# Kernel tuning notes

Hardware: AMD Instinct MI355X
Metric: run time of the kernel (lower is better)

The kernel has to match this reference:

```python
import jax, jax.numpy as jnp
import numpy as np

S, D, H, F = 4096, 1024, 16, 4096
DH = D // H  # 64
EPS = 1e-6


def _layer_norm(x, scale, bias):
    mu = jnp.mean(x, axis=-1, keepdims=True)
    var = jnp.mean(jnp.square(x - mu), axis=-1, keepdims=True)
    return (x - mu) * jax.lax.rsqrt(var + EPS) * scale + bias


def setup_inputs() -> dict:
    key = jax.random.key(0)
    ks = jax.random.split(key, 12)
    s = 0.02
    return {
        "x": jax.random.normal(ks[0], (S, D), jnp.float32),
        "Wq": jax.random.normal(ks[1], (D, H, DH), jnp.float32) * s,
        "bq": jnp.zeros((H, DH), jnp.float32),
        "Wk": jax.random.normal(ks[2], (D, H, DH), jnp.float32) * s,
        "bk": jnp.zeros((H, DH), jnp.float32),
        "Wv": jax.random.normal(ks[3], (D, H, DH), jnp.float32) * s,
        "bv": jnp.zeros((H, DH), jnp.float32),
        "Wo": jax.random.normal(ks[4], (H, DH, D), jnp.float32) * s,
        "bo": jnp.zeros((D,), jnp.float32),
        "ln1_scale": jnp.ones((D,), jnp.float32),
        "ln1_bias": jnp.zeros((D,), jnp.float32),
        "ln2_scale": jnp.ones((D,), jnp.float32),
        "ln2_bias": jnp.zeros((D,), jnp.float32),
        "W1": jax.random.normal(ks[5], (D, F), jnp.float32) * s,
        "b1": jnp.zeros((F,), jnp.float32),
        "W2": jax.random.normal(ks[6], (F, D), jnp.float32) * s,
        "b2": jnp.zeros((D,), jnp.float32),
    }


def reference(x, Wq, bq, Wk, bk, Wv, bv, Wo, bo,
              ln1_scale, ln1_bias, ln2_scale, ln2_bias,
              W1, b1, W2, b2):
    # --- attention block (pre-LN, no mask, no dropout, no RoPE) ---
    y = _layer_norm(x, ln1_scale, ln1_bias)            # [S, D]
    q = jnp.einsum("sd,dhk->shk", y, Wq) + bq          # [S, H, DH]
    k = jnp.einsum("sd,dhk->shk", y, Wk) + bk
    v = jnp.einsum("sd,dhk->shk", y, Wv) + bv
    scale = jnp.float32(1.0 / np.sqrt(DH))
    scores = jnp.einsum("qhd,khd->hqk", q * scale, k)  # [H, S, S]
    w = jax.nn.softmax(scores, axis=-1)
    ctx = jnp.einsum("hqk,khd->qhd", w, v)             # [S, H, DH]
    attn_out = jnp.einsum("qhd,hdo->qo", ctx, Wo) + bo  # [S, D]
    x = x + attn_out
    # --- FFN block ---
    y = _layer_norm(x, ln2_scale, ln2_bias)
    y = jax.nn.gelu(y @ W1 + b1, approximate=False)
    y = y @ W2 + b2
    return x + y
```

## Files before the change

### kernel.cpp

```cpp
#include <hip/hip_runtime.h>
#include <cstdint>
#include <cstddef>


typedef __attribute__((ext_vector_type(8))) __bf16 bf16x8;
typedef __attribute__((ext_vector_type(4))) float f32x4;
typedef __attribute__((ext_vector_type(2))) float f32x2;
typedef __attribute__((ext_vector_type(16))) float f32x16;
typedef __attribute__((ext_vector_type(4))) unsigned int u32x4;

__device__ inline unsigned short f2bf(float f) {
  unsigned int u = __float_as_uint(f);
  u += 0x7fffu + ((u >> 16) & 1u);
  return (unsigned short)(u >> 16);
}

__device__ inline void gload_lds16(const unsigned short* g, unsigned short* l) {
  __builtin_amdgcn_global_load_lds(
      (const __attribute__((address_space(1))) void*)g,
      (__attribute__((address_space(3))) void*)l, 16, 0, 0);
}

__global__ __launch_bounds__(256) void transpose_cvt(const float* __restrict__ in,
                                                     unsigned short* __restrict__ out,
                                                     int K, int N) {
  __shared__ float t[32][33];
  int nb = blockIdx.x * 32, kb = blockIdx.y * 32;
  int tx = threadIdx.x & 31, ty = threadIdx.x >> 5;
#pragma unroll
  for (int i = 0; i < 32; i += 8)
    t[ty + i][tx] = in[(size_t)(kb + ty + i) * N + nb + tx];
  __syncthreads();
#pragma unroll
  for (int i = 0; i < 32; i += 8)
    out[(size_t)(nb + ty + i) * K + kb + tx] = f2bf(t[tx][ty + i]);
}

__global__ __launch_bounds__(256) void concat3(const float* __restrict__ a,
                                               const float* __restrict__ b,
                                               const float* __restrict__ c,
                                               float* __restrict__ out) {
  int i = blockIdx.x * 256 + threadIdx.x;
  float v = (i < 1024) ? a[i] : (i < 2048 ? b[i - 1024] : c[i - 2048]);
  out[i] = v;
}

__global__ __launch_bounds__(256) void ln_kernel(const float* __restrict__ x,
                                                 const float* __restrict__ gamma,
                                                 const float* __restrict__ beta,
                                                 unsigned short* __restrict__ y) {
  int row = blockIdx.x, tid = threadIdx.x;
  const float4 v = ((const float4*)(x + (size_t)row * 1024))[tid];
  float s = v.x + v.y + v.z + v.w;
#pragma unroll
  for (int off = 1; off < 64; off <<= 1) s += __shfl_xor(s, off);
  __shared__ float red1[4], red2[4];
  int wave = tid >> 6;
  if ((tid & 63) == 0) red1[wave] = s;
  __syncthreads();
  float mu = (red1[0] + red1[1] + red1[2] + red1[3]) * (1.0f / 1024.0f);
  float dx = v.x - mu, dy = v.y - mu, dz = v.z - mu, dw = v.w - mu;
  float s2 = dx * dx + dy * dy + dz * dz + dw * dw;
#pragma unroll
  for (int off = 1; off < 64; off <<= 1) s2 += __shfl_xor(s2, off);
  if ((tid & 63) == 0) red2[wave] = s2;
  __syncthreads();
  float var = (red2[0] + red2[1] + red2[2] + red2[3]) * (1.0f / 1024.0f);
  float inv = rsqrtf(var + 1e-6f);
  int c = tid * 4;
  ushort4 o;
  o.x = f2bf(dx * inv * gamma[c + 0] + beta[c + 0]);
  o.y = f2bf(dy * inv * gamma[c + 1] + beta[c + 1]);
  o.z = f2bf(dz * inv * gamma[c + 2] + beta[c + 2]);
  o.w = f2bf(dw * inv * gamma[c + 3] + beta[c + 3]);
  ((ushort4*)(y + (size_t)row * 1024))[tid] = o;
}

template <int TM, bool GELU, bool RES, bool OUTBF, bool SCALEQ>
__global__ __launch_bounds__(256) void gemm_bt(const unsigned short* __restrict__ A,
                                               const unsigned short* __restrict__ BT,
                                               const float* __restrict__ bias,
                                               const float* __restrict__ res,
                                               void* __restrict__ out,
                                               int M, int N, int K) {
  constexpr int AI = TM / 32;
  __shared__ unsigned short As[TM * 32];
  __shared__ unsigned short Bs[128 * 32];
  int bm = blockIdx.x, bn = blockIdx.y;
  int tid = threadIdx.x;
  int wave = tid >> 6, lane = tid & 63, quad = lane >> 4, l16 = lane & 15;
  int wrow = (wave >> 1) * (16 * AI), wcol = (wave & 1) * 64;
  f32x4 zero = {0.f, 0.f, 0.f, 0.f};
  f32x4 acc[AI][4];
#pragma unroll
  for (int i = 0; i < AI; i++)
#pragma unroll
    for (int j = 0; j < 4; j++) acc[i][j] = zero;

  const int srow = tid >> 2;
  const int scol = (tid & 3) * 8;
  const unsigned short* aG0 = A + (size_t)(bm * TM + srow) * K + scol;
  const unsigned short* aG1 = A + (size_t)(bm * TM + 64 + srow) * K + scol;
  const unsigned short* bG0 = BT + (size_t)(bn * 128 + srow) * K + scol;
  const unsigned short* bG1 = BT + (size_t)(bn * 128 + 64 + srow) * K + scol;
  unsigned short* aL0 = As + (size_t)tid * 8;
  unsigned short* aL1 = As + (size_t)(256 + tid) * 8;
  unsigned short* bL0 = Bs + (size_t)tid * 8;
  unsigned short* bL1 = Bs + (size_t)(256 + tid) * 8;

  for (int k0 = 0; k0 < K; k0 += 32) {
    __syncthreads();
    gload_lds16(aG0 + k0, aL0);
    if (TM == 128) gload_lds16(aG1 + k0, aL1);
    gload_lds16(bG0 + k0, bL0);
    gload_lds16(bG1 + k0, bL1);
    __syncthreads();
    bf16x8 af[AI], bfr[4];
#pragma unroll
    for (int i = 0; i < AI; i++) af[i] = *(const bf16x8*)&As[(wrow + i * 16 + l16) * 32 + quad * 8];
#pragma unroll
    for (int j = 0; j < 4; j++) bfr[j] = *(const bf16x8*)&Bs[(wcol + j * 16 + l16) * 32 + quad * 8];
#pragma unroll
    for (int i = 0; i < AI; i++)
#pragma unroll
      for (int j = 0; j < 4; j++)
        acc[i][j] = __builtin_amdgcn_mfma_f32_16x16x32_bf16(af[i], bfr[j], acc[i][j], 0, 0, 0);
  }

#pragma unroll
  for (int i = 0; i < AI; i++) {
    int row = bm * TM + wrow + i * 16 + quad * 4;
#pragma unroll
    for (int j = 0; j < 4; j++) {
      int col = bn * 128 + wcol + j * 16 + l16;
      float bv = bias[col];
      float qs = (SCALEQ && col < 1024) ? 0.18033688f : 1.0f;
#pragma unroll
      for (int r = 0; r < 4; r++) {
        float v = (acc[i][j][r] + bv) * qs;
        if (GELU) v = 0.5f * v * (1.0f + erff(v * 0.70710678118654752440f));
        if (RES) v += res[(size_t)(row + r) * N + col];
        if (OUTBF)
          ((unsigned short*)out)[(size_t)(row + r) * N + col] = f2bf(v);
        else
          ((float*)out)[(size_t)(row + r) * N + col] = v;
      }
    }
  }
}

__global__ __launch_bounds__(256) void prep_kv(const unsigned short* __restrict__ qkv,
                                               unsigned short* __restrict__ Kp,
                                               unsigned short* __restrict__ Vp) {
  __shared__ unsigned short Vt[64 * 64];
  int t = blockIdx.x, h = blockIdx.y;
  int tid = threadIdx.x;
  const int r2 = tid >> 3, c0 = (tid & 7) * 8;
  size_t tb = ((size_t)h * 64 + t) * 4096;
  {
    const unsigned short* kp = qkv + (size_t)(t * 64 + r2) * 3072 + 1024 + h * 64 + c0;
    uint4 k0 = *(const uint4*)kp;
    uint4 k1 = *(const uint4*)(kp + (size_t)32 * 3072);
    int c = c0 >> 3;
    *(uint4*)(Kp + tb + c * 512 + r2 * 8) = k0;
    *(uint4*)(Kp + tb + c * 512 + (r2 + 32) * 8) = k1;
  }
  {
    const unsigned short* vp = qkv + (size_t)(t * 64 + 2 * r2) * 3072 + 2048 + h * 64 + c0;
    uint4 v0 = *(const uint4*)vp;
    uint4 v1 = *(const uint4*)(vp + 3072);
    const unsigned short* p0 = (const unsigned short*)&v0;
    const unsigned short* p1 = (const unsigned short*)&v1;
#pragma unroll
    for (int dd = 0; dd < 8; dd++) {
      unsigned int pk = (unsigned int)p0[dd] | ((unsigned int)p1[dd] << 16);
      *(unsigned int*)&Vt[(c0 + dd) * 64 + 2 * r2] = pk;
    }
  }
  __syncthreads();
#pragma unroll
  for (int u0 = 0; u0 < 2; u0++) {
    int u = tid + u0 * 256;
    *(uint4*)(Vp + tb + u * 8) = *(const uint4*)&Vt[(u & 63) * 64 + (u >> 6) * 8];
  }
}

__global__ __launch_bounds__(256, 3) void attn_kernel(const unsigned short* __restrict__ qkv,
                                                      const unsigned short* __restrict__ Kp,
                                                      const unsigned short* __restrict__ Vp,
                                                      unsigned short* __restrict__ ctx) {
  __shared__ float comb[2 * 32 * 64];
  __shared__ float lpart[4 * 32];
  int qt = blockIdx.x, h = blockIdx.y;
  int tid = threadIdx.x;
  int w = tid >> 6, lane = tid & 63;
  int l31 = lane & 31, hi = lane >> 5;
  int qsub = w & 1, kvh = w >> 1;

  bf16x8 qf[4];
  {
    const unsigned short* qp = qkv + (size_t)(qt * 64 + qsub * 32 + l31) * 3072 + h * 64 + hi * 8;
#pragma unroll
    for (int kk = 0; kk < 4; kk++) qf[kk] = *(const bf16x8*)(qp + kk * 16);
  }

  const size_t hb = (size_t)h * 64 * 4096;
  const unsigned short* kB = Kp + hb + hi * 512 + (kvh * 32 + l31) * 8;
  const unsigned short* vB = Vp + hb + (kvh * 4 + hi) * 512 + l31 * 8;

  f32x16 accO0, accO1;
  f32x2 lp2 = {0.f, 0.f};
#pragma unroll
  for (int r = 0; r < 16; r++) { accO0[r] = 0.f; accO1[r] = 0.f; }

  bf16x8 kf[4];
#pragma unroll
  for (int kk = 0; kk < 4; kk++) kf[kk] = *(const bf16x8*)(kB + kk * 1024);

  for (int t = 0; t < 64; t++) {
    const unsigned short* vt = vB + (size_t)t * 4096;
    bf16x8 vA0 = *(const bf16x8*)(vt);
    bf16x8 vA1 = *(const bf16x8*)(vt + 1024);
    bf16x8 vB0 = *(const bf16x8*)(vt + 256);
    bf16x8 vB1 = *(const bf16x8*)(vt + 1024 + 256);

    f32x16 accS;
#pragma unroll
    for (int r = 0; r < 16; r++) accS[r] = 0.f;
#pragma unroll
    for (int kk = 0; kk < 4; kk++)
      accS = __builtin_amdgcn_mfma_f32_32x32x16_bf16(kf[kk], qf[kk], accS, 0, 0, 0);

    if (t < 63) {
      const unsigned short* kt = kB + (size_t)(t + 1) * 4096;
#pragma unroll
      for (int kk = 0; kk < 4; kk++) kf[kk] = *(const bf16x8*)(kt + kk * 1024);
    }

    unsigned int pd[8];
#pragma unroll
    for (int i = 0; i < 8; i++) {
      float a = __builtin_amdgcn_exp2f(accS[2 * i]);
      float b = __builtin_amdgcn_exp2f(accS[2 * i + 1]);
      f32x2 ab = {a, b};
      lp2 += ab;
      pd[i] = __builtin_amdgcn_perm(__float_as_uint(b), __float_as_uint(a), 0x07060302);
    }
    asm("v_permlane32_swap_b32 %0, %1" : "+v"(pd[0]), "+v"(pd[2]));
    asm("v_permlane32_swap_b32 %0, %1" : "+v"(pd[1]), "+v"(pd[3]));
    asm("v_permlane32_swap_b32 %0, %1" : "+v"(pd[4]), "+v"(pd[6]));
    asm("v_permlane32_swap_b32 %0, %1" : "+v"(pd[5]), "+v"(pd[7]));
    u32x4 f0 = {pd[0], pd[1], pd[2], pd[3]};
    u32x4 f1 = {pd[4], pd[5], pd[6], pd[7]};
    bf16x8 pa0 = __builtin_bit_cast(bf16x8, f0);
    bf16x8 pa1 = __builtin_bit_cast(bf16x8, f1);

    accO0 = __builtin_amdgcn_mfma_f32_32x32x16_bf16(pa0, vA0, accO0, 0, 0, 0);
    accO1 = __builtin_amdgcn_mfma_f32_32x32x16_bf16(pa0, vB0, accO1, 0, 0, 0);
    accO0 = __builtin_amdgcn_mfma_f32_32x32x16_bf16(pa1, vA1, accO0, 0, 0, 0);
    accO1 = __builtin_amdgcn_mfma_f32_32x32x16_bf16(pa1, vB1, accO1, 0, 0, 0);
  }

  float lp = lp2.x + lp2.y;
  lp += __shfl_xor(lp, 32);
  if (hi == 0) lpart[(kvh * 2 + qsub) * 32 + l31] = lp;
  if (kvh == 1) {
#pragma unroll
    for (int r = 0; r < 16; r++) {
      int q = (r & 3) + 8 * (r >> 2) + 4 * hi;
      comb[(qsub * 32 + q) * 64 + l31] = accO0[r];
      comb[(qsub * 32 + q) * 64 + 32 + l31] = accO1[r];
    }
  }
  __syncthreads();
  if (kvh == 0) {
#pragma unroll
    for (int r = 0; r < 16; r++) {
      int q = (r & 3) + 8 * (r >> 2) + 4 * hi;
      float l = lpart[qsub * 32 + q] + lpart[(2 + qsub) * 32 + q];
      float inv = 1.0f / l;
      float v0 = (accO0[r] + comb[(qsub * 32 + q) * 64 + l31]) * inv;
      float v1 = (accO1[r] + comb[(qsub * 32 + q) * 64 + 32 + l31]) * inv;
      int row = qt * 64 + qsub * 32 + q;
      size_t o = (size_t)row * 1024 + h * 64;
      ctx[o + l31] = f2bf(v0);
      ctx[o + 32 + l31] = f2bf(v1);
    }
  }
}

extern "C" void kernel_launch(void* const* d_in, const int* in_sizes, int n_in,
                              void* d_out, int out_size, void* d_ws, size_t ws_size,
                              hipStream_t stream) {
  const float* x   = (const float*)d_in[0];
  const float* Wq  = (const float*)d_in[1];
  const float* bq  = (const float*)d_in[2];
  const float* Wk  = (const float*)d_in[3];
  const float* bk  = (const float*)d_in[4];
  const float* Wv  = (const float*)d_in[5];
  const float* bv  = (const float*)d_in[6];
  const float* Wo  = (const float*)d_in[7];
  const float* bo  = (const float*)d_in[8];
  const float* g1  = (const float*)d_in[9];
  const float* be1 = (const float*)d_in[10];
  const float* g2  = (const float*)d_in[11];
  const float* be2 = (const float*)d_in[12];
  const float* W1  = (const float*)d_in[13];
  const float* b1  = (const float*)d_in[14];
  const float* W2  = (const float*)d_in[15];
  const float* b2  = (const float*)d_in[16];
  float* out = (float*)d_out;

  char* p = (char*)d_ws;
  unsigned short* WqkvT = (unsigned short*)p; p += (size_t)3072 * 1024 * 2;
  unsigned short* WoT   = (unsigned short*)p; p += (size_t)1024 * 1024 * 2;
  unsigned short* W1T   = (unsigned short*)p; p += (size_t)4096 * 1024 * 2;
  unsigned short* W2T   = (unsigned short*)p; p += (size_t)1024 * 4096 * 2;
  float*          bqkv  = (float*)p;          p += 16384;
  unsigned short* y1    = (unsigned short*)p; p += (size_t)4096 * 1024 * 2;
  unsigned short* qkvb  = (unsigned short*)p; p += (size_t)4096 * 3072 * 2;
  unsigned short* ctxb  = (unsigned short*)p; p += (size_t)4096 * 1024 * 2;
  float*          x1    = (float*)p;          p += (size_t)4096 * 1024 * 4;
  unsigned short* Kp    = (unsigned short*)p; p += (size_t)16 * 64 * 4096 * 2;
  unsigned short* Vp    = (unsigned short*)p; p += (size_t)16 * 64 * 4096 * 2;
  unsigned short* hbuf  = qkvb;

  dim3 b256(256);
  transpose_cvt<<<dim3(32, 32), b256, 0, stream>>>(Wq, WqkvT, 1024, 1024);
  transpose_cvt<<<dim3(32, 32), b256, 0, stream>>>(Wk, WqkvT + (size_t)1024 * 1024, 1024, 1024);
  transpose_cvt<<<dim3(32, 32), b256, 0, stream>>>(Wv, WqkvT + (size_t)2048 * 1024, 1024, 1024);
  transpose_cvt<<<dim3(32, 32), b256, 0, stream>>>(Wo, WoT, 1024, 1024);
  transpose_cvt<<<dim3(128, 32), b256, 0, stream>>>(W1, W1T, 1024, 4096);
  transpose_cvt<<<dim3(32, 128), b256, 0, stream>>>(W2, W2T, 4096, 1024);
  concat3<<<12, b256, 0, stream>>>(bq, bk, bv, bqkv);

  ln_kernel<<<4096, b256, 0, stream>>>(x, g1, be1, y1);
  gemm_bt<128, false, false, true, true><<<dim3(32, 24), b256, 0, stream>>>(y1, WqkvT, bqkv, nullptr, qkvb, 4096, 3072, 1024);
  prep_kv<<<dim3(64, 16), b256, 0, stream>>>(qkvb, Kp, Vp);
  attn_kernel<<<dim3(64, 16), b256, 0, stream>>>(qkvb, Kp, Vp, ctxb);
  gemm_bt<64, false, true, false, false><<<dim3(64, 8), b256, 0, stream>>>(ctxb, WoT, bo, x, x1, 4096, 1024, 1024);
  ln_kernel<<<4096, b256, 0, stream>>>(x1, g2, be2, y1);
  gemm_bt<128, true, false, true, false><<<dim3(32, 32), b256, 0, stream>>>(y1, W1T, b1, nullptr, hbuf, 4096, 4096, 1024);
  gemm_bt<64, false, true, false, false><<<dim3(64, 8), b256, 0, stream>>>(hbuf, W2T, b2, x1, out, 4096, 1024, 4096);
}
```

Baseline: 446.1 us.

## Replace GEMM kernel with 8-wave double-buffered swizzled large-tile GEMM

Replaces the single-buffered 256-thread GEMM with a 512-thread kernel that uses larger tiles (256x256 or 128x128) and BK=64. It double-buffers LDS so global-to-LDS prefetch of the next K slice overlaps MFMA work. LDS uses an XOR swizzle to avoid bank conflicts, and blocks are remapped for cache locality. The larger tiles and register accumulators raise register pressure and may lower occupancy. The 1D grid mapping assumes the grid divides evenly by 8.

```diff
diff --git a/kernel.cpp b/kernel.cpp
--- a/kernel.cpp
+++ b/kernel.cpp
@@ -76,74 +76,172 @@
   ((ushort4*)(y + (size_t)row * 1024))[tid] = o;
 }
 
-template <int TM, bool GELU, bool RES, bool OUTBF, bool SCALEQ>
-__global__ __launch_bounds__(256) void gemm_bt(const unsigned short* __restrict__ A,
-                                               const unsigned short* __restrict__ BT,
-                                               const float* __restrict__ bias,
-                                               const float* __restrict__ res,
-                                               void* __restrict__ out,
-                                               int M, int N, int K) {
-  constexpr int AI = TM / 32;
-  __shared__ unsigned short As[TM * 32];
-  __shared__ unsigned short Bs[128 * 32];
-  int bm = blockIdx.x, bn = blockIdx.y;
-  int tid = threadIdx.x;
-  int wave = tid >> 6, lane = tid & 63, quad = lane >> 4, l16 = lane & 15;
-  int wrow = (wave >> 1) * (16 * AI), wcol = (wave & 1) * 64;
-  f32x4 zero = {0.f, 0.f, 0.f, 0.f};
-  f32x4 acc[AI][4];
-#pragma unroll
-  for (int i = 0; i < AI; i++)
-#pragma unroll
-    for (int j = 0; j < 4; j++) acc[i][j] = zero;
-
-  const int srow = tid >> 2;
-  const int scol = (tid & 3) * 8;
-  const unsigned short* aG0 = A + (size_t)(bm * TM + srow) * K + scol;
-  const unsigned short* aG1 = A + (size_t)(bm * TM + 64 + srow) * K + scol;
-  const unsigned short* bG0 = BT + (size_t)(bn * 128 + srow) * K + scol;
-  const unsigned short* bG1 = BT + (size_t)(bn * 128 + 64 + srow) * K + scol;
-  unsigned short* aL0 = As + (size_t)tid * 8;
-  unsigned short* aL1 = As + (size_t)(256 + tid) * 8;
-  unsigned short* bL0 = Bs + (size_t)tid * 8;
-  unsigned short* bL1 = Bs + (size_t)(256 + tid) * 8;
-
-  for (int k0 = 0; k0 < K; k0 += 32) {
-    __syncthreads();
-    gload_lds16(aG0 + k0, aL0);
-    if (TM == 128) gload_lds16(aG1 + k0, aL1);
-    gload_lds16(bG0 + k0, bL0);
-    gload_lds16(bG1 + k0, bL1);
-    __syncthreads();
-    bf16x8 af[AI], bfr[4];
-#pragma unroll
-    for (int i = 0; i < AI; i++) af[i] = *(const bf16x8*)&As[(wrow + i * 16 + l16) * 32 + quad * 8];
-#pragma unroll
-    for (int j = 0; j < 4; j++) bfr[j] = *(const bf16x8*)&Bs[(wcol + j * 16 + l16) * 32 + quad * 8];
-#pragma unroll
-    for (int i = 0; i < AI; i++)
-#pragma unroll
-      for (int j = 0; j < 4; j++)
-        acc[i][j] = __builtin_amdgcn_mfma_f32_16x16x32_bf16(af[i], bfr[j], acc[i][j], 0, 0, 0);
-  }
-
-#pragma unroll
-  for (int i = 0; i < AI; i++) {
-    int row = bm * TM + wrow + i * 16 + quad * 4;
-#pragma unroll
-    for (int j = 0; j < 4; j++) {
-      int col = bn * 128 + wcol + j * 16 + l16;
-      float bv = bias[col];
-      float qs = (SCALEQ && col < 1024) ? 0.18033688f : 1.0f;
-#pragma unroll
-      for (int r = 0; r < 4; r++) {
-        float v = (acc[i][j][r] + bv) * qs;
+template <int BM, int BN, bool GELU, bool RES, bool OUTBF, bool SCALEQ>
+__global__ __launch_bounds__(512, (BM == 256 ? 2 : 4)) void gemm8(
+    const unsigned short* __restrict__ A,
+    const unsigned short* __restrict__ BT,
+    const float* __restrict__ bias,
+    const float* __restrict__ res,
+    void* __restrict__ out,
+    int M, int N, int K) {
+  constexpr int MH = BM / 64;
+  constexpr int NF = BN / 64;
+  constexpr int AU = BM / 64;
+  constexpr int BU = BN / 64;
+  constexpr int AOFF = BM * 64;
+  constexpr int SLOT = (BM + BN) * 64;
+  __shared__ unsigned short lds[2 * SLOT];
+  (void)M;
+
+  const int nbn = N / BN;
+  const int bid = blockIdx.x;
+  const int cpx = (int)gridDim.x >> 3;
+  const int swzb = (bid & 7) * cpx + (bid >> 3);
+  const int bm = swzb / nbn, bn = swzb % nbn;
+  const int tid = threadIdx.x;
+  const int lane = tid & 63, quad = lane >> 4, l16 = lane & 15;
+  const int wm = tid >> 8, wn = (tid >> 6) & 3;
+
+  const int rs = tid >> 3;
+  const int xo = ((tid & 7) ^ (rs & 7)) * 8;
+  const unsigned short* aSrc = A + (size_t)(bm * BM + rs) * K + xo;
+  const unsigned short* bSrc = BT + (size_t)(bn * BN + rs) * K + xo;
+
+  const int sw0 = (quad ^ (l16 & 7)) * 8;
+  const int sw1 = ((quad ^ 4) ^ (l16 & 7)) * 8;
+  const int aBase = (wm * (BM / 2) + l16) * 64;
+  const int bBase = (wn * (BN / 4) + l16) * 64;
+
+  f32x4 acc[2 * MH][NF];
+  const f32x4 z4 = {0.f, 0.f, 0.f, 0.f};
+#pragma unroll
+  for (int i = 0; i < 2 * MH; ++i)
+#pragma unroll
+    for (int n = 0; n < NF; ++n) acc[i][n] = z4;
+
+  const int NT = K >> 6;
+  {
+    unsigned short* dA = lds + (size_t)tid * 8;
+    unsigned short* dB = lds + AOFF + (size_t)tid * 8;
+#pragma unroll
+    for (int u = 0; u < AU; ++u) gload_lds16(aSrc + (size_t)u * 64 * K, dA + u * 4096);
+#pragma unroll
+    for (int u = 0; u < BU; ++u) gload_lds16(bSrc + (size_t)u * 64 * K, dB + u * 4096);
+  }
+
+  for (int j = 0; j < NT; ++j) {
+    const int s = j & 1;
+    asm volatile("s_waitcnt vmcnt(0) lgkmcnt(0)" ::: "memory");
+    __builtin_amdgcn_s_barrier();
+    __builtin_amdgcn_sched_barrier(0);
+    const unsigned short* As = lds + s * SLOT;
+    const unsigned short* Bs = As + AOFF;
+    unsigned short* stA = lds + (s ^ 1) * SLOT + (size_t)tid * 8;
+    unsigned short* stB = stA + AOFF;
+    const bool pre = (j + 1 < NT);
+    const int kN = (j + 1) << 6;
+
+    bf16x8 af[MH][2], bfr[NF][2];
+#pragma unroll
+    for (int mm = 0; mm < MH; ++mm) {
+      af[mm][0] = *(const bf16x8*)(As + aBase + mm * 1024 + sw0);
+      af[mm][1] = *(const bf16x8*)(As + aBase + mm * 1024 + sw1);
+    }
+#pragma unroll
+    for (int nn = 0; nn < 2; ++nn) {
+      bfr[nn][0] = *(const bf16x8*)(Bs + bBase + nn * 1024 + sw0);
+      bfr[nn][1] = *(const bf16x8*)(Bs + bBase + nn * 1024 + sw1);
+    }
+    if (pre) {
+#pragma unroll
+      for (int u = 0; u < AU; ++u)
+        gload_lds16(aSrc + (size_t)u * 64 * K + kN, stA + u * 4096);
+    }
+    __builtin_amdgcn_s_barrier();
+    __builtin_amdgcn_s_setprio(1);
+#pragma unroll
+    for (int mm = 0; mm < MH; ++mm)
+#pragma unroll
+      for (int nn = 0; nn < 2; ++nn) {
+        acc[mm][nn] = __builtin_amdgcn_mfma_f32_16x16x32_bf16(af[mm][0], bfr[nn][0], acc[mm][nn], 0, 0, 0);
+        acc[mm][nn] = __builtin_amdgcn_mfma_f32_16x16x32_bf16(af[mm][1], bfr[nn][1], acc[mm][nn], 0, 0, 0);
+      }
+    __builtin_amdgcn_s_setprio(0);
+    if constexpr (NF == 4) {
+#pragma unroll
+      for (int nn = 2; nn < 4; ++nn) {
+        bfr[nn][0] = *(const bf16x8*)(Bs + bBase + nn * 1024 + sw0);
+        bfr[nn][1] = *(const bf16x8*)(Bs + bBase + nn * 1024 + sw1);
+      }
+      if (pre) {
+#pragma unroll
+        for (int u = 0; u < BU; ++u)
+          gload_lds16(bSrc + (size_t)u * 64 * K + kN, stB + u * 4096);
+      }
+      __builtin_amdgcn_s_barrier();
+      __builtin_amdgcn_s_setprio(1);
+#pragma unroll
+      for (int mm = 0; mm < MH; ++mm)
+#pragma unroll
+        for (int nn = 2; nn < 4; ++nn) {
+          acc[mm][nn] = __builtin_amdgcn_mfma_f32_16x16x32_bf16(af[mm][0], bfr[nn][0], acc[mm][nn], 0, 0, 0);
+          acc[mm][nn] = __builtin_amdgcn_mfma_f32_16x16x32_bf16(af[mm][1], bfr[nn][1], acc[mm][nn], 0, 0, 0);
+        }
+      __builtin_amdgcn_s_setprio(0);
+    }
+#pragma unroll
+    for (int mm = 0; mm < MH; ++mm) {
+      af[mm][0] = *(const bf16x8*)(As + aBase + MH * 1024 + mm * 1024 + sw0);
+      af[mm][1] = *(const bf16x8*)(As + aBase + MH * 1024 + mm * 1024 + sw1);
+    }
+    if constexpr (NF == 2) {
+      if (pre) {
+#pragma unroll
+        for (int u = 0; u < BU; ++u)
+          gload_lds16(bSrc + (size_t)u * 64 * K + kN, stB + u * 4096);
+      }
+    }
+    __builtin_amdgcn_s_barrier();
+    __builtin_amdgcn_s_setprio(1);
+#pragma unroll
+    for (int mm = 0; mm < MH; ++mm)
+#pragma unroll
+      for (int nn = 0; nn < 2; ++nn) {
+        acc[MH + mm][nn] = __builtin_amdgcn_mfma_f32_16x16x32_bf16(af[mm][0], bfr[nn][0], acc[MH + mm][nn], 0, 0, 0);
+        acc[MH + mm][nn] = __builtin_amdgcn_mfma_f32_16x16x32_bf16(af[mm][1], bfr[nn][1], acc[MH + mm][nn], 0, 0, 0);
+      }
+    __builtin_amdgcn_s_setprio(0);
+    if constexpr (NF == 4) {
+      __builtin_amdgcn_s_barrier();
+      __builtin_amdgcn_s_setprio(1);
+#pragma unroll
+      for (int mm = 0; mm < MH; ++mm)
+#pragma unroll
+        for (int nn = 2; nn < 4; ++nn) {
+          acc[MH + mm][nn] = __builtin_amdgcn_mfma_f32_16x16x32_bf16(af[mm][0], bfr[nn][0], acc[MH + mm][nn], 0, 0, 0);
+          acc[MH + mm][nn] = __builtin_amdgcn_mfma_f32_16x16x32_bf16(af[mm][1], bfr[nn][1], acc[MH + mm][nn], 0, 0, 0);
+        }
+      __builtin_amdgcn_s_setprio(0);
+    }
+  }
+
+#pragma unroll
+  for (int mi = 0; mi < 2 * MH; ++mi) {
+    const int row0 = bm * BM + wm * (BM / 2) + mi * 16 + quad * 4;
+#pragma unroll
+    for (int ni = 0; ni < NF; ++ni) {
+      const int col = bn * BN + wn * (BN / 4) + ni * 16 + l16;
+      const float bv = bias[col];
+      const float qs = (SCALEQ && col < 1024) ? 0.18033688f : 1.0f;
+#pragma unroll
+      for (int r = 0; r < 4; ++r) {
+        float v = (acc[mi][ni][r] + bv) * qs;
         if (GELU) v = 0.5f * v * (1.0f + erff(v * 0.70710678118654752440f));
-        if (RES) v += res[(size_t)(row + r) * N + col];
+        if (RES) v += res[(size_t)(row0 + r) * N + col];
         if (OUTBF)
-          ((unsigned short*)out)[(size_t)(row + r) * N + col] = f2bf(v);
+          ((unsigned short*)out)[(size_t)(row0 + r) * N + col] = f2bf(v);
         else
-          ((float*)out)[(size_t)(row + r) * N + col] = v;
+          ((float*)out)[(size_t)(row0 + r) * N + col] = v;
       }
     }
   }
@@ -326,6 +424,7 @@
   unsigned short* hbuf  = qkvb;
 
   dim3 b256(256);
+  dim3 b512(512);
   transpose_cvt<<<dim3(32, 32), b256, 0, stream>>>(Wq, WqkvT, 1024, 1024);
   transpose_cvt<<<dim3(32, 32), b256, 0, stream>>>(Wk, WqkvT + (size_t)1024 * 1024, 1024, 1024);
   transpose_cvt<<<dim3(32, 32), b256, 0, stream>>>(Wv, WqkvT + (size_t)2048 * 1024, 1024, 1024);
@@ -335,11 +434,11 @@
   concat3<<<12, b256, 0, stream>>>(bq, bk, bv, bqkv);
 
   ln_kernel<<<4096, b256, 0, stream>>>(x, g1, be1, y1);
-  gemm_bt<128, false, false, true, true><<<dim3(32, 24), b256, 0, stream>>>(y1, WqkvT, bqkv, nullptr, qkvb, 4096, 3072, 1024);
+  gemm8<256, 256, false, false, true, true><<<dim3(192), b512, 0, stream>>>(y1, WqkvT, bqkv, nullptr, qkvb, 4096, 3072, 1024);
   prep_kv<<<dim3(64, 16), b256, 0, stream>>>(qkvb, Kp, Vp);
   attn_kernel<<<dim3(64, 16), b256, 0, stream>>>(qkvb, Kp, Vp, ctxb);
-  gemm_bt<64, false, true, false, false><<<dim3(64, 8), b256, 0, stream>>>(ctxb, WoT, bo, x, x1, 4096, 1024, 1024);
+  gemm8<128, 128, false, true, false, false><<<dim3(256), b512, 0, stream>>>(ctxb, WoT, bo, x, x1, 4096, 1024, 1024);
   ln_kernel<<<4096, b256, 0, stream>>>(x1, g2, be2, y1);
-  gemm_bt<128, true, false, true, false><<<dim3(32, 32), b256, 0, stream>>>(y1, W1T, b1, nullptr, hbuf, 4096, 4096, 1024);
-  gemm_bt<64, false, true, false, false><<<dim3(64, 8), b256, 0, stream>>>(hbuf, W2T, b2, x1, out, 4096, 1024, 4096);
-}
+  gemm8<256, 256, true, false, true, false><<<dim3(256), b512, 0, stream>>>(y1, W1T, b1, nullptr, hbuf, 4096, 4096, 1024);
+  gemm8<128, 128, false, true, false, false><<<dim3(256), b512, 0, stream>>>(hbuf, W2T, b2, x1, out, 4096, 1024, 4096);
+}
```

After: 390.3 us. 12.5% less time.
